# Performance work log

Hardware: AMD Instinct MI355X
Metric: run time of the kernel (lower is better)

Reference implementation:

```python
import jax, jax.numpy as jnp
import numpy as np

N_NODES = 50000
N_EDGES = 800000
D_FEAT = 32
J = 4
NUM_GRAPHS = 64
MAX_SCALE = 2 ** (J - 1)  # 8 diffusion steps


def _propagate(x, src, dst, w):
    # gather x_j, weight per-edge, scatter-add into target nodes
    msgs = x[src] * w[:, None]
    return jax.ops.segment_sum(msgs, dst, num_segments=N_NODES)


def _diffuse(x, src, dst, w):
    outs = []
    x_curr = x
    for step in range(1, MAX_SCALE + 1):
        x_curr = _propagate(x_curr, src, dst, w)
        if step & (step - 1) == 0:  # collect at powers of two: 1,2,4,8 -> J scales
            outs.append(x_curr)
    return outs


def setup_inputs() -> dict:
    key = jax.random.key(0)
    k1, k2, k3, k4 = jax.random.split(key, 4)
    X = jax.random.normal(k1, (N_NODES, D_FEAT), dtype=jnp.float32)
    edge_index = jax.random.randint(k2, (2, N_EDGES), 0, N_NODES, dtype=jnp.int64)
    edge_weight = jax.random.uniform(k3, (N_EDGES,), dtype=jnp.float32)
    batch = jnp.sort(jax.random.randint(k4, (N_NODES,), 0, NUM_GRAPHS, dtype=jnp.int64))
    return {"X": X, "edge_index": edge_index, "edge_weight": edge_weight, "batch": batch}


def reference(X, edge_index, edge_weight, batch):
    src, dst = edge_index[0], edge_index[1]
    diff_list = _diffuse(X, src, dst, edge_weight)
    # F0: deepest scale
    F0 = diff_list[-1]
    # F1: first-order wavelet coefficients |psi_j x|
    F1 = jnp.concatenate(
        [jnp.abs(diff_list[i - 1] - diff_list[i]) for i in range(1, len(diff_list))],
        axis=1,
    )
    # F2: second-order, diffuse concatenated scales once more
    U = jnp.concatenate(diff_list, axis=1)  # [N, J*d]
    U_diff = _diffuse(U, src, dst, edge_weight)
    res = []
    for j in range(J):
        cs, ce = j * D_FEAT, (j + 1) * D_FEAT
        for jp in range(j + 1, J):
            res.append(jnp.abs(U_diff[jp][:, cs:ce] - U_diff[jp - 1][:, cs:ce]))
    F2 = jnp.concatenate(res, axis=1)
    feats = jnp.concatenate([F0, F1, F2], axis=1)  # [N, d*(1 + (J-1) + J*(J-1)/2)] = [N, 320]
    # global_mean_pool over batch assignment
    sums = jax.ops.segment_sum(feats, batch, num_segments=NUM_GRAPHS)
    counts = jax.ops.segment_sum(jnp.ones((feats.shape[0],), feats.dtype), batch, num_segments=NUM_GRAPHS)
    return sums / jnp.maximum(counts, 1.0)[:, None]
```

## Files before the change

kernel.cpp:

```cpp
#include <hip/hip_runtime.h>

#define N_NODES 50000
#define N_EDGES 800000
#define D_FEAT 32
#define NUM_GRAPHS 64
#define FEATS 320
#define NBIN 128
#define BINSH 9
#define CE 4096
#define NCHUNK ((N_EDGES + CE - 1) / CE)
#define NPB ((N_NODES + 511) / 512)

__device__ __forceinline__ unsigned short f2bf(float f) {
    unsigned int u = __float_as_uint(f);
    u = (u + 0x7fffu + ((u >> 16) & 1u)) >> 16;
    return (unsigned short)u;
}
__device__ __forceinline__ float bf2f(unsigned short h) {
    return __uint_as_float((unsigned int)h << 16);
}


__global__ void binA_kernel(const int* __restrict__ dst, int* __restrict__ counts, int n) {
    __shared__ int h[NBIN];
    int t = threadIdx.x;
    if (t < NBIN) h[t] = 0;
    __syncthreads();
    int s0 = blockIdx.x * CE, e0 = min(s0 + CE, n);
    for (int i = s0 + t; i < e0; i += blockDim.x)
        atomicAdd(&h[dst[i] >> BINSH], 1);
    __syncthreads();
    if (t < NBIN) counts[blockIdx.x * NBIN + t] = h[t];
}

__global__ void binB_kernel(int* __restrict__ counts, int* __restrict__ binBase) {
    __shared__ int s[NBIN];
    int b = threadIdx.x;
    int tot = 0;
    #pragma unroll 8
    for (int c = 0; c < NCHUNK; ++c) tot += counts[c * NBIN + b];
    s[b] = tot;
    __syncthreads();
    for (int off = 1; off < NBIN; off <<= 1) {
        int u = (b >= off) ? s[b - off] : 0;
        __syncthreads();
        s[b] += u;
        __syncthreads();
    }
    int base = s[b] - tot;
    binBase[b] = base;
    if (b == NBIN - 1) binBase[NBIN] = s[b];
    int running = base;
    #pragma unroll 4
    for (int c = 0; c < NCHUNK; ++c) {
        int idx = c * NBIN + b;
        int v = counts[idx];
        counts[idx] = running;
        running += v;
    }
}

__global__ __launch_bounds__(256) void binC_kernel(const int* __restrict__ src,
                                                   const int* __restrict__ dst,
                                                   const float* __restrict__ w,
                                                   const int* __restrict__ counts,
                                                   int2* __restrict__ tmp, int n) {
    __shared__ int h[NBIN], sc[NBIN], cur[NBIN], gbase[NBIN];
    __shared__ int2 srec[CE];
    __shared__ unsigned char sbin[CE];
    int t = threadIdx.x;
    if (t < NBIN) h[t] = 0;
    __syncthreads();
    int s0 = blockIdx.x * CE, e0 = min(s0 + CE, n);
    int cnt = e0 - s0;
    for (int i = s0 + t; i < e0; i += blockDim.x)
        atomicAdd(&h[dst[i] >> BINSH], 1);
    __syncthreads();
    if (t < NBIN) sc[t] = h[t];
    __syncthreads();
    for (int off = 1; off < NBIN; off <<= 1) {
        int u = (t < NBIN && t >= off) ? sc[t - off] : 0;
        __syncthreads();
        if (t < NBIN) sc[t] += u;
        __syncthreads();
    }
    if (t < NBIN) {
        cur[t] = 0;
        gbase[t] = counts[blockIdx.x * NBIN + t];
    }
    __syncthreads();
    for (int i = s0 + t; i < e0; i += blockDim.x) {
        int d = dst[i];
        int b = d >> BINSH;
        int pos = (sc[b] - h[b]) + atomicAdd(&cur[b], 1);
        srec[pos] = make_int2(src[i] | ((int)f2bf(w[i]) << 16), d & 511);
        sbin[pos] = (unsigned char)b;
    }
    __syncthreads();
    for (int j = t; j < cnt; j += blockDim.x) {
        int b = sbin[j];
        tmp[gbase[b] + (j - (sc[b] - h[b]))] = srec[j];
    }
}

__global__ __launch_bounds__(256) void place_kernel(const int* __restrict__ binBase,
                                                    const int2* __restrict__ tmp,
                                                    unsigned int* __restrict__ edges,
                                                    int* __restrict__ rowptr, int n) {
    __shared__ int h[512], sc[512], cur[512];
    int b = blockIdx.x;
    int t = threadIdx.x;
    int base = binBase[b], end = binBase[b + 1];
    for (int i = t; i < 512; i += 256) { h[i] = 0; cur[i] = 0; }
    __syncthreads();
    for (int e = base + t; e < end; e += 256)
        atomicAdd(&h[tmp[e].y], 1);
    __syncthreads();
    for (int i = t; i < 512; i += 256) sc[i] = h[i];
    __syncthreads();
    for (int off = 1; off < 512; off <<= 1) {
        int i0 = t, i1 = t + 256;
        int a0 = (i0 >= off) ? sc[i0 - off] : 0;
        int a1 = (i1 >= off) ? sc[i1 - off] : 0;
        __syncthreads();
        sc[i0] += a0;
        sc[i1] += a1;
        __syncthreads();
    }
    int node0 = b << BINSH;
    for (int i = t; i < 512; i += 256) {
        int node = node0 + i;
        if (node <= n) rowptr[node] = base + sc[i] - h[i];
    }
    if (b == 0 && t == 0) rowptr[0] = 0;
    __syncthreads();
    for (int e = base + t; e < end; e += 256) {
        int2 p = tmp[e];
        int loc = p.y;
        int pos = base + (sc[loc] - h[loc]) + atomicAdd(&cur[loc], 1);
        edges[pos] = (unsigned int)p.x;
    }
}


__global__ void prep_kernel(const float4* __restrict__ xin, ushort4* __restrict__ xout,
                            const int* __restrict__ batch, int* __restrict__ gstart, int n) {
    int i = blockIdx.x * blockDim.x + threadIdx.x;
    if (i < n * 8) {
        float4 v = xin[i];
        ushort4 o;
        o.x = f2bf(v.x); o.y = f2bf(v.y); o.z = f2bf(v.z); o.w = f2bf(v.w);
        xout[i] = o;
    }
    if (i < n) {
        int g = batch[i];
        int gp = (i == 0) ? -1 : batch[i - 1];
        for (int gg = gp + 1; gg <= g; ++gg) gstart[gg] = i;
        if (i == n - 1)
            for (int gg = g + 1; gg <= NUM_GRAPHS; ++gg) gstart[gg] = n;
    }
}


__global__ __launch_bounds__(256) void spmm_kernel(const ushort4* __restrict__ xin,
                                                   ushort4* __restrict__ yout,
                                                   const int* __restrict__ rowptr,
                                                   const unsigned int* __restrict__ edges,
                                                   int n) {
    int lane = threadIdx.x & 7;
    int node = (blockIdx.x * blockDim.x + threadIdx.x) >> 3;
    if (node >= n) return;
    int e0 = rowptr[node], e1 = rowptr[node + 1];
    float a0 = 0.f, a1 = 0.f, a2 = 0.f, a3 = 0.f;
    int e = e0;
    int e8 = e0 + ((e1 - e0) & ~7);
    for (; e < e8; e += 8) {
        unsigned int r[8];
        #pragma unroll
        for (int u = 0; u < 8; ++u) r[u] = edges[e + u];
        ushort4 v[8];
        #pragma unroll
        for (int u = 0; u < 8; ++u)
            v[u] = xin[(size_t)(r[u] & 0xffff) * 8 + lane];
        #pragma unroll
        for (int u = 0; u < 8; ++u) {
            float w = bf2f((unsigned short)(r[u] >> 16));
            a0 += bf2f(v[u].x) * w;
            a1 += bf2f(v[u].y) * w;
            a2 += bf2f(v[u].z) * w;
            a3 += bf2f(v[u].w) * w;
        }
    }
    for (; e < e1; ++e) {
        unsigned int r = edges[e];
        ushort4 v = xin[(size_t)(r & 0xffff) * 8 + lane];
        float w = bf2f((unsigned short)(r >> 16));
        a0 += bf2f(v.x) * w; a1 += bf2f(v.y) * w; a2 += bf2f(v.z) * w; a3 += bf2f(v.w) * w;
    }
    yout[(size_t)node * 8 + lane] = make_ushort4(f2bf(a0), f2bf(a1), f2bf(a2), f2bf(a3));
}


struct PoolArgs10 {
    const unsigned short* P[10];
    const unsigned short* Q[10];
};

__global__ __launch_bounds__(320) void pool_kernel(PoolArgs10 a, const int* __restrict__ gstart,
                                                   float* __restrict__ out) {
    int k = threadIdx.x >> 5;
    int f = threadIdx.x & 31;
    int g = blockIdx.x >> 4;
    int s = blockIdx.x & 15;
    int gs = gstart[g], ge = gstart[g + 1];
    int len = ge - gs;
    int i0 = gs + ((len * s) >> 4);
    int i1 = gs + ((len * (s + 1)) >> 4);
    const unsigned short* __restrict__ P = a.P[k];
    const unsigned short* __restrict__ Q = a.Q[k];
    float acc = 0.f;
    if (Q) {
        for (int i = i0; i < i1; ++i)
            acc += fabsf(bf2f(P[(size_t)i * 32 + f]) - bf2f(Q[(size_t)i * 32 + f]));
    } else {
        for (int i = i0; i < i1; ++i)
            acc += bf2f(P[(size_t)i * 32 + f]);
    }
    if (i1 > i0) {
        float inv = 1.0f / (float)max(len, 1);
        atomicAdd(&out[g * FEATS + k * 32 + f], acc * inv);
    }
}


extern "C" void kernel_launch(void* const* d_in, const int* in_sizes, int n_in,
                              void* d_out, int out_size, void* d_ws, size_t ws_size,
                              hipStream_t stream) {
    const float* X     = (const float*)d_in[0];
    const int*   ei    = (const int*)d_in[1];
    const float* ew    = (const float*)d_in[2];
    const int*   batch = (const int*)d_in[3];
    float* out = (float*)d_out;

    const int N = N_NODES, E = N_EDGES;
    const int* src = ei;
    const int* dst = ei + E;

    char* base = (char*)d_ws;
    size_t off = 0;
    auto alloc = [&](size_t bytes) -> void* {
        void* p = base + off;
        off += (bytes + 255) & ~(size_t)255;
        return p;
    };
    unsigned short* y[13];
    for (int k = 0; k <= 12; ++k) y[k] = (unsigned short*)alloc((size_t)N * 32 * 2);

    int*  rowptr  = (int*)alloc((size_t)(N + 4) * 4);
    int*  gstart  = (int*)alloc((NUM_GRAPHS + 1) * 4);
    int*  counts  = (int*)alloc((size_t)NCHUNK * NBIN * 4);
    int*  binBase = (int*)alloc((NBIN + 1) * 4);
    int2* tmp     = (int2*)alloc((size_t)E * 8);
    unsigned int* edges = (unsigned int*)alloc((size_t)E * 4);

    hipMemsetAsync(out, 0, (size_t)out_size * 4, stream);

    binA_kernel<<<NCHUNK, 256, 0, stream>>>(dst, counts, E);
    binB_kernel<<<1, NBIN, 0, stream>>>(counts, binBase);
    binC_kernel<<<NCHUNK, 256, 0, stream>>>(src, dst, ew, counts, tmp, E);
    place_kernel<<<NPB, 256, 0, stream>>>(binBase, tmp, edges, rowptr, N);

    prep_kernel<<<(N * 8 + 255) / 256, 256, 0, stream>>>((const float4*)X, (ushort4*)y[0],
                                                         batch, gstart, N);

    const int SPMM_GRID = (N * 8 + 255) / 256;
    for (int k = 1; k <= 12; ++k) {
        spmm_kernel<<<SPMM_GRID, 256, 0, stream>>>((const ushort4*)y[k - 1], (ushort4*)y[k],
                                                   rowptr, edges, N);
    }

    {
        PoolArgs10 p{};
        const unsigned short* Ps[10] = {y[8], y[1], y[2], y[4], y[3], y[5], y[9], y[6], y[10], y[12]};
        const unsigned short* Qs[10] = {nullptr, y[2], y[4], y[8], y[2], y[3], y[5], y[4], y[6], y[8]};
        for (int k = 0; k < 10; ++k) { p.P[k] = Ps[k]; p.Q[k] = Qs[k]; }
        pool_kernel<<<NUM_GRAPHS * 16, 320, 0, stream>>>(p, gstart, out);
    }
}
```

Baseline: 291.6 us.

## Quantize node features to int8 with per-node scales across diffusion chain

Node feature tensors switch from bf16 to 8-bit offset-quantized values with one float scale per node. Each SpMM dequantizes neighbour rows on the fly, folding the scale into the edge weight and subtracting the offset through a weight sum. It then requantizes its output using a max reduction across the 8 lanes of each node. The aim is to halve the gather bytes in the twelve memory-bound SpMM passes, at the cost of an extra scale load per edge and accumulated quantization error that may break accuracy tolerance.

```diff
diff --git a/kernel.cpp b/kernel.cpp
--- a/kernel.cpp
+++ b/kernel.cpp
@@ -20,6 +20,11 @@
     return __uint_as_float((unsigned int)h << 16);
 }
 
+__device__ __forceinline__ unsigned int pack8(int q0, int q1, int q2, int q3) {
+    return (unsigned int)(q0 & 0xff) | ((unsigned int)(q1 & 0xff) << 8) |
+           ((unsigned int)(q2 & 0xff) << 16) | ((unsigned int)(q3 & 0xff) << 24);
+}
+
 
 __global__ void binA_kernel(const int* __restrict__ dst, int* __restrict__ counts, int n) {
     __shared__ int h[NBIN];
@@ -143,14 +148,23 @@
 }
 
 
-__global__ void prep_kernel(const float4* __restrict__ xin, ushort4* __restrict__ xout,
+__global__ void prep_kernel(const float4* __restrict__ xin, unsigned int* __restrict__ xout,
+                            float* __restrict__ xsc,
                             const int* __restrict__ batch, int* __restrict__ gstart, int n) {
     int i = blockIdx.x * blockDim.x + threadIdx.x;
     if (i < n * 8) {
         float4 v = xin[i];
-        ushort4 o;
-        o.x = f2bf(v.x); o.y = f2bf(v.y); o.z = f2bf(v.z); o.w = f2bf(v.w);
-        xout[i] = o;
+        float m = fmaxf(fmaxf(fabsf(v.x), fabsf(v.y)), fmaxf(fabsf(v.z), fabsf(v.w)));
+        m = fmaxf(m, __shfl_xor(m, 1, 8));
+        m = fmaxf(m, __shfl_xor(m, 2, 8));
+        m = fmaxf(m, __shfl_xor(m, 4, 8));
+        float inv = (m > 1e-30f) ? 127.f / m : 0.f;
+        int q0 = __float2int_rn(v.x * inv) + 127;
+        int q1 = __float2int_rn(v.y * inv) + 127;
+        int q2 = __float2int_rn(v.z * inv) + 127;
+        int q3 = __float2int_rn(v.w * inv) + 127;
+        xout[i] = pack8(q0, q1, q2, q3);
+        if ((i & 7) == 0) xsc[i >> 3] = (m > 1e-30f) ? m * (1.f / 127.f) : 0.f;
     }
     if (i < n) {
         int g = batch[i];
@@ -162,8 +176,10 @@
 }
 
 
-__global__ __launch_bounds__(256) void spmm_kernel(const ushort4* __restrict__ xin,
-                                                   ushort4* __restrict__ yout,
+__global__ __launch_bounds__(256) void spmm_kernel(const unsigned int* __restrict__ xin,
+                                                   const float* __restrict__ xsc,
+                                                   unsigned int* __restrict__ yout,
+                                                   float* __restrict__ ysc,
                                                    const int* __restrict__ rowptr,
                                                    const unsigned int* __restrict__ edges,
                                                    int n) {
@@ -171,39 +187,62 @@
     int node = (blockIdx.x * blockDim.x + threadIdx.x) >> 3;
     if (node >= n) return;
     int e0 = rowptr[node], e1 = rowptr[node + 1];
-    float a0 = 0.f, a1 = 0.f, a2 = 0.f, a3 = 0.f;
+    float a0 = 0.f, a1 = 0.f, a2 = 0.f, a3 = 0.f, wacc = 0.f;
     int e = e0;
     int e8 = e0 + ((e1 - e0) & ~7);
     for (; e < e8; e += 8) {
         unsigned int r[8];
         #pragma unroll
         for (int u = 0; u < 8; ++u) r[u] = edges[e + u];
-        ushort4 v[8];
-        #pragma unroll
-        for (int u = 0; u < 8; ++u)
-            v[u] = xin[(size_t)(r[u] & 0xffff) * 8 + lane];
+        unsigned int v[8];
+        float s[8];
         #pragma unroll
         for (int u = 0; u < 8; ++u) {
-            float w = bf2f((unsigned short)(r[u] >> 16));
-            a0 += bf2f(v[u].x) * w;
-            a1 += bf2f(v[u].y) * w;
-            a2 += bf2f(v[u].z) * w;
-            a3 += bf2f(v[u].w) * w;
+            int srcn = (int)(r[u] & 0xffffu);
+            v[u] = xin[(size_t)srcn * 8 + lane];
+            s[u] = xsc[srcn];
+        }
+        #pragma unroll
+        for (int u = 0; u < 8; ++u) {
+            float w = bf2f((unsigned short)(r[u] >> 16)) * s[u];
+            wacc += w;
+            a0 += (float)(v[u] & 0xffu) * w;
+            a1 += (float)((v[u] >> 8) & 0xffu) * w;
+            a2 += (float)((v[u] >> 16) & 0xffu) * w;
+            a3 += (float)(v[u] >> 24) * w;
         }
     }
     for (; e < e1; ++e) {
         unsigned int r = edges[e];
-        ushort4 v = xin[(size_t)(r & 0xffff) * 8 + lane];
-        float w = bf2f((unsigned short)(r >> 16));
-        a0 += bf2f(v.x) * w; a1 += bf2f(v.y) * w; a2 += bf2f(v.z) * w; a3 += bf2f(v.w) * w;
-    }
-    yout[(size_t)node * 8 + lane] = make_ushort4(f2bf(a0), f2bf(a1), f2bf(a2), f2bf(a3));
+        int srcn = (int)(r & 0xffffu);
+        unsigned int v = xin[(size_t)srcn * 8 + lane];
+        float w = bf2f((unsigned short)(r >> 16)) * xsc[srcn];
+        wacc += w;
+        a0 += (float)(v & 0xffu) * w;
+        a1 += (float)((v >> 8) & 0xffu) * w;
+        a2 += (float)((v >> 16) & 0xffu) * w;
+        a3 += (float)(v >> 24) * w;
+    }
+    a0 -= 127.f * wacc; a1 -= 127.f * wacc; a2 -= 127.f * wacc; a3 -= 127.f * wacc;
+    float m = fmaxf(fmaxf(fabsf(a0), fabsf(a1)), fmaxf(fabsf(a2), fabsf(a3)));
+    m = fmaxf(m, __shfl_xor(m, 1, 8));
+    m = fmaxf(m, __shfl_xor(m, 2, 8));
+    m = fmaxf(m, __shfl_xor(m, 4, 8));
+    float inv = (m > 1e-30f) ? 127.f / m : 0.f;
+    int q0 = __float2int_rn(a0 * inv) + 127;
+    int q1 = __float2int_rn(a1 * inv) + 127;
+    int q2 = __float2int_rn(a2 * inv) + 127;
+    int q3 = __float2int_rn(a3 * inv) + 127;
+    yout[(size_t)node * 8 + lane] = pack8(q0, q1, q2, q3);
+    if (lane == 0) ysc[node] = (m > 1e-30f) ? m * (1.f / 127.f) : 0.f;
 }
 
 
 struct PoolArgs10 {
-    const unsigned short* P[10];
-    const unsigned short* Q[10];
+    const unsigned char* P[10];
+    const unsigned char* Q[10];
+    const float* PS[10];
+    const float* QS[10];
 };
 
 __global__ __launch_bounds__(320) void pool_kernel(PoolArgs10 a, const int* __restrict__ gstart,
@@ -216,19 +255,24 @@
     int len = ge - gs;
     int i0 = gs + ((len * s) >> 4);
     int i1 = gs + ((len * (s + 1)) >> 4);
-    const unsigned short* __restrict__ P = a.P[k];
-    const unsigned short* __restrict__ Q = a.Q[k];
+    const unsigned char* __restrict__ P = a.P[k];
+    const unsigned char* __restrict__ Q = a.Q[k];
+    const float* __restrict__ PS = a.PS[k];
+    const float* __restrict__ QS = a.QS[k];
     float acc = 0.f;
     if (Q) {
-        for (int i = i0; i < i1; ++i)
-            acc += fabsf(bf2f(P[(size_t)i * 32 + f]) - bf2f(Q[(size_t)i * 32 + f]));
+        for (int i = i0; i < i1; ++i) {
+            float p = ((float)P[(size_t)i * 32 + f] - 127.f) * PS[i];
+            float q = ((float)Q[(size_t)i * 32 + f] - 127.f) * QS[i];
+            acc += fabsf(p - q);
+        }
     } else {
         for (int i = i0; i < i1; ++i)
-            acc += bf2f(P[(size_t)i * 32 + f]);
+            acc += ((float)P[(size_t)i * 32 + f] - 127.f) * PS[i];
     }
     if (i1 > i0) {
-        float inv = 1.0f / (float)max(len, 1);
-        atomicAdd(&out[g * FEATS + k * 32 + f], acc * inv);
+        float invl = 1.0f / (float)max(len, 1);
+        atomicAdd(&out[g * FEATS + k * 32 + f], acc * invl);
     }
 }
 
@@ -253,8 +297,12 @@
         off += (bytes + 255) & ~(size_t)255;
         return p;
     };
-    unsigned short* y[13];
-    for (int k = 0; k <= 12; ++k) y[k] = (unsigned short*)alloc((size_t)N * 32 * 2);
+    unsigned char* y[13];
+    float* sc[13];
+    for (int k = 0; k <= 12; ++k) {
+        y[k]  = (unsigned char*)alloc((size_t)N * 32);
+        sc[k] = (float*)alloc((size_t)N * 4);
+    }
 
     int*  rowptr  = (int*)alloc((size_t)(N + 4) * 4);
     int*  gstart  = (int*)alloc((NUM_GRAPHS + 1) * 4);
@@ -270,20 +318,26 @@
     binC_kernel<<<NCHUNK, 256, 0, stream>>>(src, dst, ew, counts, tmp, E);
     place_kernel<<<NPB, 256, 0, stream>>>(binBase, tmp, edges, rowptr, N);
 
-    prep_kernel<<<(N * 8 + 255) / 256, 256, 0, stream>>>((const float4*)X, (ushort4*)y[0],
-                                                         batch, gstart, N);
+    prep_kernel<<<(N * 8 + 255) / 256, 256, 0, stream>>>((const float4*)X, (unsigned int*)y[0],
+                                                         sc[0], batch, gstart, N);
 
     const int SPMM_GRID = (N * 8 + 255) / 256;
     for (int k = 1; k <= 12; ++k) {
-        spmm_kernel<<<SPMM_GRID, 256, 0, stream>>>((const ushort4*)y[k - 1], (ushort4*)y[k],
+        spmm_kernel<<<SPMM_GRID, 256, 0, stream>>>((const unsigned int*)y[k - 1], sc[k - 1],
+                                                   (unsigned int*)y[k], sc[k],
                                                    rowptr, edges, N);
     }
 
     {
         PoolArgs10 p{};
-        const unsigned short* Ps[10] = {y[8], y[1], y[2], y[4], y[3], y[5], y[9], y[6], y[10], y[12]};
-        const unsigned short* Qs[10] = {nullptr, y[2], y[4], y[8], y[2], y[3], y[5], y[4], y[6], y[8]};
-        for (int k = 0; k < 10; ++k) { p.P[k] = Ps[k]; p.Q[k] = Qs[k]; }
+        const int Pi[10] = {8, 1, 2, 4, 3, 5, 9, 6, 10, 12};
+        const int Qi[10] = {-1, 2, 4, 8, 2, 3, 5, 4, 6, 8};
+        for (int k = 0; k < 10; ++k) {
+            p.P[k]  = y[Pi[k]];
+            p.PS[k] = sc[Pi[k]];
+            p.Q[k]  = (Qi[k] < 0) ? nullptr : y[Qi[k]];
+            p.QS[k] = (Qi[k] < 0) ? nullptr : sc[Qi[k]];
+        }
         pool_kernel<<<NUM_GRAPHS * 16, 320, 0, stream>>>(p, gstart, out);
     }
 }
```

Result: slower. 298.9 us (+2.5%).

## Widen SpMM gathers to 16-byte loads and deduplicate pooling reads

Applied to the files above, without the earlier changes.

The SpMM kernel now uses 4 lanes per node with uint4 (8 bf16) loads instead of 8 lanes with ushort4. It unrolls the edge loop 16 deep with a 4-edge remainder loop, and adds a launch-bounds occupancy hint. The pool kernel now reads each of the 10 distinct diffusion buffers once per node instead of up to twice. It reduces partial sums across 8 row-groups in shared memory before issuing atomics. The trade-offs are higher register pressure in SpMM and fewer threads overall per node.

```diff
diff --git a/kernel.cpp b/kernel.cpp
--- a/kernel.cpp
+++ b/kernel.cpp
@@ -19,6 +19,8 @@
 __device__ __forceinline__ float bf2f(unsigned short h) {
     return __uint_as_float((unsigned int)h << 16);
 }
+__device__ __forceinline__ float bflo(unsigned int u) { return __uint_as_float(u << 16); }
+__device__ __forceinline__ float bfhi(unsigned int u) { return __uint_as_float(u & 0xffff0000u); }
 
 
 __global__ void binA_kernel(const int* __restrict__ dst, int* __restrict__ counts, int n) {
@@ -162,73 +164,113 @@
 }
 
 
-__global__ __launch_bounds__(256) void spmm_kernel(const ushort4* __restrict__ xin,
-                                                   ushort4* __restrict__ yout,
-                                                   const int* __restrict__ rowptr,
-                                                   const unsigned int* __restrict__ edges,
-                                                   int n) {
-    int lane = threadIdx.x & 7;
-    int node = (blockIdx.x * blockDim.x + threadIdx.x) >> 3;
+__global__ __launch_bounds__(256, 4) void spmm_kernel(const uint4* __restrict__ xin,
+                                                      uint4* __restrict__ yout,
+                                                      const int* __restrict__ rowptr,
+                                                      const unsigned int* __restrict__ edges,
+                                                      int n) {
+    int lane = threadIdx.x & 3;
+    int node = (blockIdx.x * blockDim.x + threadIdx.x) >> 2;
     if (node >= n) return;
     int e0 = rowptr[node], e1 = rowptr[node + 1];
     float a0 = 0.f, a1 = 0.f, a2 = 0.f, a3 = 0.f;
+    float a4 = 0.f, a5 = 0.f, a6 = 0.f, a7 = 0.f;
     int e = e0;
-    int e8 = e0 + ((e1 - e0) & ~7);
-    for (; e < e8; e += 8) {
-        unsigned int r[8];
-        #pragma unroll
-        for (int u = 0; u < 8; ++u) r[u] = edges[e + u];
-        ushort4 v[8];
-        #pragma unroll
-        for (int u = 0; u < 8; ++u)
-            v[u] = xin[(size_t)(r[u] & 0xffff) * 8 + lane];
-        #pragma unroll
-        for (int u = 0; u < 8; ++u) {
-            float w = bf2f((unsigned short)(r[u] >> 16));
-            a0 += bf2f(v[u].x) * w;
-            a1 += bf2f(v[u].y) * w;
-            a2 += bf2f(v[u].z) * w;
-            a3 += bf2f(v[u].w) * w;
+    int e16 = e0 + ((e1 - e0) & ~15);
+    for (; e < e16; e += 16) {
+        unsigned int r[16];
+        #pragma unroll
+        for (int u = 0; u < 16; ++u) r[u] = edges[e + u];
+        uint4 v[16];
+        #pragma unroll
+        for (int u = 0; u < 16; ++u)
+            v[u] = xin[(size_t)(r[u] & 0xffffu) * 4 + lane];
+        #pragma unroll
+        for (int u = 0; u < 16; ++u) {
+            float w = bfhi(r[u]);
+            a0 += bflo(v[u].x) * w; a1 += bfhi(v[u].x) * w;
+            a2 += bflo(v[u].y) * w; a3 += bfhi(v[u].y) * w;
+            a4 += bflo(v[u].z) * w; a5 += bfhi(v[u].z) * w;
+            a6 += bflo(v[u].w) * w; a7 += bfhi(v[u].w) * w;
+        }
+    }
+    int e4 = e0 + ((e1 - e0) & ~3);
+    for (; e < e4; e += 4) {
+        unsigned int r[4];
+        #pragma unroll
+        for (int u = 0; u < 4; ++u) r[u] = edges[e + u];
+        uint4 v[4];
+        #pragma unroll
+        for (int u = 0; u < 4; ++u)
+            v[u] = xin[(size_t)(r[u] & 0xffffu) * 4 + lane];
+        #pragma unroll
+        for (int u = 0; u < 4; ++u) {
+            float w = bfhi(r[u]);
+            a0 += bflo(v[u].x) * w; a1 += bfhi(v[u].x) * w;
+            a2 += bflo(v[u].y) * w; a3 += bfhi(v[u].y) * w;
+            a4 += bflo(v[u].z) * w; a5 += bfhi(v[u].z) * w;
+            a6 += bflo(v[u].w) * w; a7 += bfhi(v[u].w) * w;
         }
     }
     for (; e < e1; ++e) {
         unsigned int r = edges[e];
-        ushort4 v = xin[(size_t)(r & 0xffff) * 8 + lane];
-        float w = bf2f((unsigned short)(r >> 16));
-        a0 += bf2f(v.x) * w; a1 += bf2f(v.y) * w; a2 += bf2f(v.z) * w; a3 += bf2f(v.w) * w;
-    }
-    yout[(size_t)node * 8 + lane] = make_ushort4(f2bf(a0), f2bf(a1), f2bf(a2), f2bf(a3));
-}
-
-
-struct PoolArgs10 {
-    const unsigned short* P[10];
-    const unsigned short* Q[10];
-};
-
-__global__ __launch_bounds__(320) void pool_kernel(PoolArgs10 a, const int* __restrict__ gstart,
+        uint4 v = xin[(size_t)(r & 0xffffu) * 4 + lane];
+        float w = bfhi(r);
+        a0 += bflo(v.x) * w; a1 += bfhi(v.x) * w;
+        a2 += bflo(v.y) * w; a3 += bfhi(v.y) * w;
+        a4 += bflo(v.z) * w; a5 += bfhi(v.z) * w;
+        a6 += bflo(v.w) * w; a7 += bfhi(v.w) * w;
+    }
+    uint4 o;
+    o.x = (unsigned int)f2bf(a0) | ((unsigned int)f2bf(a1) << 16);
+    o.y = (unsigned int)f2bf(a2) | ((unsigned int)f2bf(a3) << 16);
+    o.z = (unsigned int)f2bf(a4) | ((unsigned int)f2bf(a5) << 16);
+    o.w = (unsigned int)f2bf(a6) | ((unsigned int)f2bf(a7) << 16);
+    yout[(size_t)node * 4 + lane] = o;
+}
+
+
+struct PoolPtrs { const unsigned short* a[10]; };
+
+__global__ __launch_bounds__(256) void pool_kernel(PoolPtrs P, const int* __restrict__ gstart,
                                                    float* __restrict__ out) {
-    int k = threadIdx.x >> 5;
-    int f = threadIdx.x & 31;
+    __shared__ float red[8][FEATS];
+    int t = threadIdx.x;
+    int f = t & 31;
+    int sub = t >> 5;
     int g = blockIdx.x >> 4;
     int s = blockIdx.x & 15;
     int gs = gstart[g], ge = gstart[g + 1];
     int len = ge - gs;
     int i0 = gs + ((len * s) >> 4);
     int i1 = gs + ((len * (s + 1)) >> 4);
-    const unsigned short* __restrict__ P = a.P[k];
-    const unsigned short* __restrict__ Q = a.Q[k];
-    float acc = 0.f;
-    if (Q) {
-        for (int i = i0; i < i1; ++i)
-            acc += fabsf(bf2f(P[(size_t)i * 32 + f]) - bf2f(Q[(size_t)i * 32 + f]));
-    } else {
-        for (int i = i0; i < i1; ++i)
-            acc += bf2f(P[(size_t)i * 32 + f]);
-    }
-    if (i1 > i0) {
-        float inv = 1.0f / (float)max(len, 1);
-        atomicAdd(&out[g * FEATS + k * 32 + f], acc * inv);
+    float acc[10];
+    #pragma unroll
+    for (int k = 0; k < 10; ++k) acc[k] = 0.f;
+    for (int i = i0 + sub; i < i1; i += 8) {
+        float v[10];
+        #pragma unroll
+        for (int k = 0; k < 10; ++k) v[k] = bf2f(P.a[k][(size_t)i * 32 + f]);
+        acc[0] += v[6];
+        acc[1] += fabsf(v[0] - v[1]);
+        acc[2] += fabsf(v[1] - v[3]);
+        acc[3] += fabsf(v[3] - v[6]);
+        acc[4] += fabsf(v[2] - v[1]);
+        acc[5] += fabsf(v[4] - v[2]);
+        acc[6] += fabsf(v[7] - v[4]);
+        acc[7] += fabsf(v[5] - v[3]);
+        acc[8] += fabsf(v[8] - v[5]);
+        acc[9] += fabsf(v[9] - v[6]);
+    }
+    #pragma unroll
+    for (int k = 0; k < 10; ++k) red[sub][k * 32 + f] = acc[k];
+    __syncthreads();
+    float invl = 1.0f / (float)max(len, 1);
+    for (int o = t; o < FEATS; o += 256) {
+        float ssum = 0.f;
+        #pragma unroll
+        for (int j = 0; j < 8; ++j) ssum += red[j][o];
+        if (ssum != 0.f || true) atomicAdd(&out[g * FEATS + o], ssum * invl);
     }
 }
 
@@ -273,17 +315,16 @@
     prep_kernel<<<(N * 8 + 255) / 256, 256, 0, stream>>>((const float4*)X, (ushort4*)y[0],
                                                          batch, gstart, N);
 
-    const int SPMM_GRID = (N * 8 + 255) / 256;
+    const int SPMM_GRID = (N * 4 + 255) / 256;
     for (int k = 1; k <= 12; ++k) {
-        spmm_kernel<<<SPMM_GRID, 256, 0, stream>>>((const ushort4*)y[k - 1], (ushort4*)y[k],
+        spmm_kernel<<<SPMM_GRID, 256, 0, stream>>>((const uint4*)y[k - 1], (uint4*)y[k],
                                                    rowptr, edges, N);
     }
 
     {
-        PoolArgs10 p{};
-        const unsigned short* Ps[10] = {y[8], y[1], y[2], y[4], y[3], y[5], y[9], y[6], y[10], y[12]};
-        const unsigned short* Qs[10] = {nullptr, y[2], y[4], y[8], y[2], y[3], y[5], y[4], y[6], y[8]};
-        for (int k = 0; k < 10; ++k) { p.P[k] = Ps[k]; p.Q[k] = Qs[k]; }
-        pool_kernel<<<NUM_GRAPHS * 16, 320, 0, stream>>>(p, gstart, out);
-    }
-}
+        PoolPtrs p;
+        const int idx[10] = {1, 2, 3, 4, 5, 6, 8, 9, 10, 12};
+        for (int k = 0; k < 10; ++k) p.a[k] = y[idx[k]];
+        pool_kernel<<<NUM_GRAPHS * 16, 256, 0, stream>>>(p, gstart, out);
+    }
+}
```

Result: faster. 267.9 us (-8.1%).
